# Kernel optimization log

Measured on AMD Instinct MI355X. Metric: run time of the kernel, lower is better.

The kernel has to match this reference:

```python
import jax, jax.numpy as jnp
import numpy as np
from jax import lax

N_GRAPHS = 256
N_NODES = 128      # nodes per graph (fixed-size batching)
N_TPLT = 16
N_TPLT_NODES = 10
N_FEAT = 128
AVG_DEG = 8
EPS = 0.1          # entropic regularization for the GW solver
OUTER_ITERS = 5    # outer mirror-descent (entropic GW) iterations
SINKHORN_ITERS = 20


def setup_inputs() -> dict:
    key = jax.random.key(0)
    k1, k2, k3, k4, k5 = jax.random.split(key, 5)
    x = jax.random.normal(k1, (N_GRAPHS * N_NODES, N_FEAT), jnp.float32)
    # per-graph random edges with global node ids (PyG convention)
    n_e = N_NODES * AVG_DEG
    src = jax.random.randint(k2, (N_GRAPHS, n_e), 0, N_NODES)
    dst = jax.random.randint(k3, (N_GRAPHS, n_e), 0, N_NODES)
    off = (jnp.arange(N_GRAPHS) * N_NODES)[:, None]
    edge_index = jnp.stack([(src + off).reshape(-1), (dst + off).reshape(-1)]).astype(jnp.int32)
    batch = jnp.repeat(jnp.arange(N_GRAPHS, dtype=jnp.int32), N_NODES)
    # template parameters (symmetric uniform adjacencies, normal features, zero q0 -> uniform weights)
    A0 = jax.random.uniform(k4, (N_TPLT, N_TPLT_NODES, N_TPLT_NODES), jnp.float32)
    tplt_adjacencies = 0.5 * (A0 + jnp.swapaxes(A0, 1, 2))
    tplt_features = jax.random.normal(k5, (N_TPLT, N_TPLT_NODES, N_FEAT), jnp.float32)
    q0 = jnp.zeros((N_TPLT, N_TPLT_NODES), jnp.float32)
    return {"x": x, "edge_index": edge_index, "batch": batch,
            "tplt_adjacencies": tplt_adjacencies, "tplt_features": tplt_features, "q0": q0}


def _gw_distances(C1, C2, p, q):
    # C1: [B,N,N] graph adjacencies, C2: [T,M,M] templates, p: [N], q: [T,M]
    # square-loss GW decomposition (Peyre et al.): f1=a^2, f2=b^2, h1=a, h2=2b
    B, N = C1.shape[0], C1.shape[1]
    T, M = C2.shape[0], C2.shape[1]
    f1p = jnp.einsum('bij,j->bi', C1 * C1, p)          # [B,N]
    f2q = jnp.einsum('tij,tj->ti', C2 * C2, q)         # [T,M]
    constC = f1p[:, None, :, None] + f2q[None, :, None, :]  # [B,T,N,M]

    def tens(P):
        # constC - h1(C1) P h2(C2)^T
        cross = jnp.einsum('bik,btkm,tjm->btij', C1, P, 2.0 * C2)
        return constC - cross

    P0 = jnp.broadcast_to(p[None, None, :, None] * q[None, :, None, :], (B, T, N, M))

    def outer(P, _):
        cost = 2.0 * tens(P)                     # GW gradient
        K = jnp.exp(-cost / EPS)                 # [B,T,N,M]
        u0 = jnp.ones((B, T, N), K.dtype)
        v0 = jnp.ones((B, T, M), K.dtype)

        def inner(carry, _):
            u, v = carry
            u = p[None, None, :] / jnp.einsum('btnm,btm->btn', K, v)
            v = q[None, :, :] / jnp.einsum('btnm,btn->btm', K, u)
            return (u, v), None

        (u, v), _ = lax.scan(inner, (u0, v0), None, length=SINKHORN_ITERS)
        P = u[..., :, None] * K * v[..., None, :]
        return P, None

    P, _ = lax.scan(outer, P0, None, length=OUTER_ITERS)
    return jnp.sum(tens(P) * P, axis=(2, 3))     # [B,T]


def reference(x, edge_index, batch, tplt_adjacencies, tplt_features, q0):
    # q = softmax(q0, dim=1): template node weights
    q = jax.nn.softmax(q0, axis=1)
    # dense per-graph adjacency from the sparse edge list
    g = batch[edge_index[0]]
    src = edge_index[0] - g * N_NODES
    dst = edge_index[1] - g * N_NODES
    C1 = jnp.zeros((N_GRAPHS, N_NODES, N_NODES), x.dtype)
    C1 = C1.at[g, src, dst].set(1.0)
    C1 = jnp.maximum(C1, jnp.swapaxes(C1, 1, 2))  # undirected
    p = jnp.full((N_NODES,), 1.0 / N_NODES, x.dtype)  # uniform graph node weights
    # fused=False: pure Gromov-Wasserstein, node features are not used
    return _gw_distances(C1, tplt_adjacencies, p, q)
```

## Files before the change

### kernel.cpp

```cpp
#include <hip/hip_runtime.h>

#define NGRAPH 256
#define NN     128
#define NT     16
#define NM     10
#define OUTER_IT 5
#define SINK_IT  20

#define SC1  28.85390081777927f
#define SC2  57.70780163555854f

typedef unsigned long long u64;
typedef float v2f __attribute__((ext_vector_type(2)));
typedef float v4f __attribute__((ext_vector_type(4)));

static __device__ __forceinline__ v2f pkfma(v2f a, v2f b, v2f c) {
  return __builtin_elementwise_fma(a, b, c);
}
static __device__ __forceinline__ v2f bc2(float s) { return (v2f){s, s}; }

template <int CTRL>
__device__ __forceinline__ float dpp_add(float a) {
  int t = __builtin_amdgcn_update_dpp(0, __float_as_int(a), CTRL, 0xf, 0xf, true);
  return a + __int_as_float(t);
}
__device__ __forceinline__ float allsum32(float x) {
  x = dpp_add<0xB1>(x);
  x = dpp_add<0x4E>(x);
  x = dpp_add<0x141>(x);
  x = dpp_add<0x140>(x);
  int sw = __builtin_amdgcn_ds_swizzle(__float_as_int(x), 0x401F);
  return x + __int_as_float(sw);
}

__global__ __launch_bounds__(64, 2)
void tgw_kernel(const int* __restrict__ ei,
                const float* __restrict__ tadj,
                const float* __restrict__ q0g,
                float* __restrict__ out,
                int E, int ne) {
  const int lane = threadIdx.x;
  const int p    = lane >> 5;
  const int sub  = lane & 31;
  const int b    = blockIdx.x >> 3;
  const int t0   = (blockIdx.x & 7) * 2;

  __shared__ __align__(16) unsigned adj[NN][4];
  __shared__ __align__(16) float Pls[2][NN][12];
  __shared__ __align__(16) v2f C2T[2][NM][6];
  __shared__ float q0s[2][NM];

  for (int i = lane; i < NN * 4; i += 64) (&adj[0][0])[i] = 0u;
  for (int i = lane; i < 2 * NM * 5; i += 64) {
    int tt = i / 50, r = i % 50, m = r / 5, jp = r % 5;
    const float* bp = tadj + (t0 + tt) * NM * NM + m;
    C2T[tt][m][jp] = (v2f){bp[(2 * jp) * NM], bp[(2 * jp + 1) * NM]} * SC2;
  }
  if (lane < 2 * NM) q0s[lane / NM][lane % NM] = q0g[t0 * NM + lane];
  __syncthreads();

  const int* srcp = ei;
  const int* dstp = ei + E;
  const int ebase = b * ne;
  for (int e = lane; e < ne; e += 64) {
    int s = srcp[ebase + e] & (NN - 1);
    int d = dstp[ebase + e] & (NN - 1);
    atomicOr(&adj[s][d >> 5], 1u << (d & 31));
    atomicOr(&adj[d][s >> 5], 1u << (s & 31));
  }
  __syncthreads();

  float qv[NM];
  {
    float mx = q0s[p][0];
    #pragma unroll
    for (int j = 1; j < NM; ++j) mx = fmaxf(mx, q0s[p][j]);
    float s = 0.f;
    #pragma unroll
    for (int j = 0; j < NM; ++j) { qv[j] = __expf(q0s[p][j] - mx); s += qv[j]; }
    float inv = __builtin_amdgcn_rcpf(s);
    #pragma unroll
    for (int j = 0; j < NM; ++j) qv[j] *= inv;
  }
  v2f q2[5];
  #pragma unroll
  for (int jp = 0; jp < 5; ++jp) q2[jp] = (v2f){qv[2 * jp], qv[2 * jp + 1]};

  v2f fq2[5], qC2T[5];
  {
    #pragma unroll
    for (int jp = 0; jp < 5; ++jp) { fq2[jp] = (v2f){0.f, 0.f}; qC2T[jp] = (v2f){0.f, 0.f}; }
    #pragma unroll
    for (int m = 0; m < NM; ++m) {
      v2f qb = bc2(qv[m]);
      #pragma unroll
      for (int jp = 0; jp < 5; ++jp) {
        v2f c = C2T[p][m][jp];
        fq2[jp]  = pkfma(c * c, qb, fq2[jp]);
        qC2T[jp] = pkfma(c, qb, qC2T[jp]);
      }
    }
    const float f = -1.0f / (4.0f * SC1);
    #pragma unroll
    for (int jp = 0; jp < 5; ++jp) fq2[jp] *= f;
  }

  const float pw = 1.0f / 128.0f;
  float f1p[4], m1f1[4];
  #pragma unroll
  for (int c = 0; c < 4; ++c) {
    uint4 mm = *(const uint4*)&adj[sub + 32 * c][0];
    u64 m0 = mm.x | ((u64)mm.y << 32), m1 = mm.z | ((u64)mm.w << 32);
    f1p[c]  = (float)(__popcll(m0) + __popcll(m1)) * pw;
    m1f1[c] = -SC1 * f1p[c];
  }

  const float* Pbase = &Pls[p][0][0];
  auto gatherRow = [&](int r, v2f* S2) {
    uint4 mm = *(const uint4*)&adj[r][0];
    u64 m0 = mm.x | ((u64)mm.y << 32), m1 = mm.z | ((u64)mm.w << 32);
    #pragma unroll
    for (int h = 0; h < 5; ++h) S2[h] = (v2f){0.f, 0.f};
    while (m0) {
      int k = (int)__builtin_ctzll(m0); m0 &= m0 - 1;
      const float* row = Pbase + k * 12;
      v4f A = *(const v4f*)row;
      v4f B = *(const v4f*)(row + 4);
      v2f C = *(const v2f*)(row + 8);
      S2[0] += A.xy; S2[1] += A.zw; S2[2] += B.xy; S2[3] += B.zw; S2[4] += C;
    }
    while (m1) {
      int k = 64 + (int)__builtin_ctzll(m1); m1 &= m1 - 1;
      const float* row = Pbase + k * 12;
      v4f A = *(const v4f*)row;
      v4f B = *(const v4f*)(row + 4);
      v2f C = *(const v2f*)(row + 8);
      S2[0] += A.xy; S2[1] += A.zw; S2[2] += B.xy; S2[3] += B.zw; S2[4] += C;
    }
  };

  auto costFromS = [&](float Sm[4][NM], v2f arg2[4][5]) {
    #pragma unroll
    for (int c = 0; c < 4; ++c) {
      v2f ib = fq2[0] + bc2(m1f1[c]);
      arg2[c][0] = ib;
      #pragma unroll
      for (int jp = 1; jp < 5; ++jp) arg2[c][jp] = fq2[jp] + bc2(m1f1[c]);
    }
    #pragma unroll
    for (int m = 0; m < NM; ++m) {
      v4f X = *(const v4f*)&C2T[p][m][0];
      v4f Y = *(const v4f*)&C2T[p][m][2];
      v2f Z = *(const v2f*)&C2T[p][m][4];
      #pragma unroll
      for (int c = 0; c < 4; ++c) {
        v2f sb = bc2(Sm[c][m]);
        arg2[c][0] = pkfma(sb, X.xy, arg2[c][0]);
        arg2[c][1] = pkfma(sb, X.zw, arg2[c][1]);
        arg2[c][2] = pkfma(sb, Y.xy, arg2[c][2]);
        arg2[c][3] = pkfma(sb, Y.zw, arg2[c][3]);
        arg2[c][4] = pkfma(sb, Z,    arg2[c][4]);
      }
    }
  };

  v2f K2[4][5], v2[5], arg2[4][5];
  float uu[4];

  for (int o = 0; o < OUTER_IT; ++o) {
    if (o == 0) {
      #pragma unroll
      for (int c = 0; c < 4; ++c) {
        v2f fb = bc2(f1p[c]);
        v2f ob = bc2(m1f1[c]);
        #pragma unroll
        for (int jp = 0; jp < 5; ++jp)
          arg2[c][jp] = pkfma(fb, qC2T[jp], fq2[jp] + ob);
      }
    } else {
      float Sm[4][NM];
      #pragma unroll
      for (int c = 0; c < 4; ++c) {
        v2f S2[5];
        gatherRow(sub + 32 * c, S2);
        #pragma unroll
        for (int h = 0; h < 5; ++h) { Sm[c][2 * h] = S2[h].x; Sm[c][2 * h + 1] = S2[h].y; }
      }
      costFromS(Sm, arg2);
    }
    #pragma unroll
    for (int c = 0; c < 4; ++c)
      #pragma unroll
      for (int jp = 0; jp < 5; ++jp)
        K2[c][jp] = (v2f){exp2f(arg2[c][jp].x), exp2f(arg2[c][jp].y)};

    #pragma unroll
    for (int jp = 0; jp < 5; ++jp) v2[jp] = (v2f){1.f, 1.f};
    for (int it = 0; it < SINK_IT; ++it) {
      #pragma unroll
      for (int c = 0; c < 4; ++c) {
        v2f d2 = K2[c][0] * v2[0];
        d2 = pkfma(K2[c][1], v2[1], d2);
        d2 = pkfma(K2[c][2], v2[2], d2);
        d2 = pkfma(K2[c][3], v2[3], d2);
        d2 = pkfma(K2[c][4], v2[4], d2);
        uu[c] = pw * __builtin_amdgcn_rcpf(d2.x + d2.y);
      }
      #pragma unroll
      for (int jp = 0; jp < 5; ++jp) {
        v2f w2 = K2[0][jp] * bc2(uu[0]);
        w2 = pkfma(K2[1][jp], bc2(uu[1]), w2);
        w2 = pkfma(K2[2][jp], bc2(uu[2]), w2);
        w2 = pkfma(K2[3][jp], bc2(uu[3]), w2);
        float cx = allsum32(w2.x);
        float cy = allsum32(w2.y);
        v2[jp] = (v2f){q2[jp].x * __builtin_amdgcn_rcpf(cx),
                       q2[jp].y * __builtin_amdgcn_rcpf(cy)};
      }
    }

    __syncthreads();
    #pragma unroll
    for (int c = 0; c < 4; ++c) {
      v2f ub = bc2(uu[c]);
      v2f x0 = K2[c][0] * ub * v2[0];
      v2f x1 = K2[c][1] * ub * v2[1];
      v2f x2 = K2[c][2] * ub * v2[2];
      v2f x3 = K2[c][3] * ub * v2[3];
      v2f x4 = K2[c][4] * ub * v2[4];
      float* row = &Pls[p][sub + 32 * c][0];
      *(v4f*)row       = (v4f){x0.x, x0.y, x1.x, x1.y};
      *(v4f*)(row + 4) = (v4f){x2.x, x2.y, x3.x, x3.y};
      *(v2f*)(row + 8) = x4;
    }
    __syncthreads();
  }

  float acc = 0.f;
  {
    float Sm[4][NM];
    #pragma unroll
    for (int c = 0; c < 4; ++c) {
      v2f S2[5];
      gatherRow(sub + 32 * c, S2);
      #pragma unroll
      for (int h = 0; h < 5; ++h) { Sm[c][2 * h] = S2[h].x; Sm[c][2 * h + 1] = S2[h].y; }
    }
    costFromS(Sm, arg2);
    const v2f nf = bc2(-1.0f / SC1);
    v2f acc2 = (v2f){0.f, 0.f};
    #pragma unroll
    for (int c = 0; c < 4; ++c) {
      v2f ub = bc2(uu[c]);
      #pragma unroll
      for (int jp = 0; jp < 5; ++jp) {
        v2f Pv = K2[c][jp] * ub * v2[jp];
        acc2 = pkfma(arg2[c][jp] * nf, Pv, acc2);
      }
    }
    acc = acc2.x + acc2.y;
  }
  float total = allsum32(acc);
  if (sub == 0) out[b * NT + t0 + p] = total;
}

extern "C" void kernel_launch(void* const* d_in, const int* in_sizes, int n_in,
                              void* d_out, int out_size, void* d_ws, size_t ws_size,
                              hipStream_t stream) {
  const int* ei   = (const int*)d_in[1];
  const float* c2 = (const float*)d_in[3];
  const float* q0 = (const float*)d_in[5];
  float* out      = (float*)d_out;
  const int E  = in_sizes[1] / 2;
  const int ne = E / NGRAPH;
  tgw_kernel<<<dim3(NGRAPH * 8), dim3(64), 0, stream>>>(ei, c2, q0, out, E, ne);
}
```

Measured before the change: 200.5 us.

## Assign one template per 64-lane block, two rows per lane, wave-wide reduction

Each block previously handled two templates, one per 32-lane half-wave with four rows per lane. Now each block handles one template, each lane owns two rows, and the Sinkhorn column sums use a full 64-lane DPP reduction with readlane. This roughly halves per-lane register state and the serial Sinkhorn work per lane, and launch bounds are raised to allow more waves per SIMD. In exchange it doubles the grid and the per-graph adjacency construction (edge atomics are repeated once per template), and the 64-lane reduction is longer.

```diff
diff --git a/kernel.cpp b/kernel.cpp
--- a/kernel.cpp
+++ b/kernel.cpp
@@ -24,39 +24,42 @@
   int t = __builtin_amdgcn_update_dpp(0, __float_as_int(a), CTRL, 0xf, 0xf, true);
   return a + __int_as_float(t);
 }
-__device__ __forceinline__ float allsum32(float x) {
-  x = dpp_add<0xB1>(x);
-  x = dpp_add<0x4E>(x);
-  x = dpp_add<0x141>(x);
-  x = dpp_add<0x140>(x);
-  int sw = __builtin_amdgcn_ds_swizzle(__float_as_int(x), 0x401F);
-  return x + __int_as_float(sw);
-}
-
-__global__ __launch_bounds__(64, 2)
+__device__ __forceinline__ float allsum64(float x) {
+  x = dpp_add<0x111>(x);
+  x = dpp_add<0x112>(x);
+  x = dpp_add<0x114>(x);
+  x = dpp_add<0x118>(x);
+  x = dpp_add<0x142>(x);
+  x = dpp_add<0x143>(x);
+  return __int_as_float(__builtin_amdgcn_readlane(__float_as_int(x), 63));
+}
+
+__global__ __launch_bounds__(64, 4)
 void tgw_kernel(const int* __restrict__ ei,
                 const float* __restrict__ tadj,
                 const float* __restrict__ q0g,
                 float* __restrict__ out,
                 int E, int ne) {
   const int lane = threadIdx.x;
-  const int p    = lane >> 5;
-  const int sub  = lane & 31;
-  const int b    = blockIdx.x >> 3;
-  const int t0   = (blockIdx.x & 7) * 2;
+  const int b    = blockIdx.x >> 4;
+  const int t    = blockIdx.x & 15;
 
   __shared__ __align__(16) unsigned adj[NN][4];
-  __shared__ __align__(16) float Pls[2][NN][12];
-  __shared__ __align__(16) v2f C2T[2][NM][6];
-  __shared__ float q0s[2][NM];
-
-  for (int i = lane; i < NN * 4; i += 64) (&adj[0][0])[i] = 0u;
-  for (int i = lane; i < 2 * NM * 5; i += 64) {
-    int tt = i / 50, r = i % 50, m = r / 5, jp = r % 5;
-    const float* bp = tadj + (t0 + tt) * NM * NM + m;
-    C2T[tt][m][jp] = (v2f){bp[(2 * jp) * NM], bp[(2 * jp + 1) * NM]} * SC2;
-  }
-  if (lane < 2 * NM) q0s[lane / NM][lane % NM] = q0g[t0 * NM + lane];
+  __shared__ __align__(16) float Pls[NN][12];
+  __shared__ __align__(16) v2f C2T[NM][6];
+  __shared__ float q0s[NM];
+
+  {
+    uint4 z = {0u, 0u, 0u, 0u};
+    ((uint4*)adj)[lane]      = z;
+    ((uint4*)adj)[lane + 64] = z;
+  }
+  if (lane < NM * 5) {
+    int m = lane / 5, jp = lane % 5;
+    const float* bp = tadj + t * NM * NM + m;
+    C2T[m][jp] = (v2f){bp[(2 * jp) * NM], bp[(2 * jp + 1) * NM]} * SC2;
+  }
+  if (lane < NM) q0s[lane] = q0g[t * NM + lane];
   __syncthreads();
 
   const int* srcp = ei;
@@ -70,21 +73,20 @@
   }
   __syncthreads();
 
-  float qv[NM];
-  {
-    float mx = q0s[p][0];
-    #pragma unroll
-    for (int j = 1; j < NM; ++j) mx = fmaxf(mx, q0s[p][j]);
+  v2f q2[5];
+  {
+    float qv[NM];
+    float mx = q0s[0];
+    #pragma unroll
+    for (int j = 1; j < NM; ++j) mx = fmaxf(mx, q0s[j]);
     float s = 0.f;
     #pragma unroll
-    for (int j = 0; j < NM; ++j) { qv[j] = __expf(q0s[p][j] - mx); s += qv[j]; }
+    for (int j = 0; j < NM; ++j) { qv[j] = __expf(q0s[j] - mx); s += qv[j]; }
     float inv = __builtin_amdgcn_rcpf(s);
     #pragma unroll
-    for (int j = 0; j < NM; ++j) qv[j] *= inv;
-  }
-  v2f q2[5];
-  #pragma unroll
-  for (int jp = 0; jp < 5; ++jp) q2[jp] = (v2f){qv[2 * jp], qv[2 * jp + 1]};
+    for (int jp = 0; jp < 5; ++jp)
+      q2[jp] = (v2f){qv[2 * jp] * inv, qv[2 * jp + 1] * inv};
+  }
 
   v2f fq2[5], qC2T[5];
   {
@@ -92,10 +94,11 @@
     for (int jp = 0; jp < 5; ++jp) { fq2[jp] = (v2f){0.f, 0.f}; qC2T[jp] = (v2f){0.f, 0.f}; }
     #pragma unroll
     for (int m = 0; m < NM; ++m) {
-      v2f qb = bc2(qv[m]);
+      float qm = (m & 1) ? q2[m >> 1].y : q2[m >> 1].x;
+      v2f qb = bc2(qm);
       #pragma unroll
       for (int jp = 0; jp < 5; ++jp) {
-        v2f c = C2T[p][m][jp];
+        v2f c = C2T[m][jp];
         fq2[jp]  = pkfma(c * c, qb, fq2[jp]);
         qC2T[jp] = pkfma(c, qb, qC2T[jp]);
       }
@@ -106,16 +109,15 @@
   }
 
   const float pw = 1.0f / 128.0f;
-  float f1p[4], m1f1[4];
+  float f1p[2], m1f1[2];
   #pragma unroll
-  for (int c = 0; c < 4; ++c) {
-    uint4 mm = *(const uint4*)&adj[sub + 32 * c][0];
+  for (int c = 0; c < 2; ++c) {
+    uint4 mm = *(const uint4*)&adj[lane + 64 * c][0];
     u64 m0 = mm.x | ((u64)mm.y << 32), m1 = mm.z | ((u64)mm.w << 32);
     f1p[c]  = (float)(__popcll(m0) + __popcll(m1)) * pw;
     m1f1[c] = -SC1 * f1p[c];
   }
 
-  const float* Pbase = &Pls[p][0][0];
   auto gatherRow = [&](int r, v2f* S2) {
     uint4 mm = *(const uint4*)&adj[r][0];
     u64 m0 = mm.x | ((u64)mm.y << 32), m1 = mm.z | ((u64)mm.w << 32);
@@ -123,7 +125,7 @@
     for (int h = 0; h < 5; ++h) S2[h] = (v2f){0.f, 0.f};
     while (m0) {
       int k = (int)__builtin_ctzll(m0); m0 &= m0 - 1;
-      const float* row = Pbase + k * 12;
+      const float* row = &Pls[k][0];
       v4f A = *(const v4f*)row;
       v4f B = *(const v4f*)(row + 4);
       v2f C = *(const v2f*)(row + 8);
@@ -131,7 +133,7 @@
     }
     while (m1) {
       int k = 64 + (int)__builtin_ctzll(m1); m1 &= m1 - 1;
-      const float* row = Pbase + k * 12;
+      const float* row = &Pls[k][0];
       v4f A = *(const v4f*)row;
       v4f B = *(const v4f*)(row + 4);
       v2f C = *(const v2f*)(row + 8);
@@ -139,22 +141,20 @@
     }
   };
 
-  auto costFromS = [&](float Sm[4][NM], v2f arg2[4][5]) {
-    #pragma unroll
-    for (int c = 0; c < 4; ++c) {
-      v2f ib = fq2[0] + bc2(m1f1[c]);
-      arg2[c][0] = ib;
-      #pragma unroll
-      for (int jp = 1; jp < 5; ++jp) arg2[c][jp] = fq2[jp] + bc2(m1f1[c]);
-    }
+  auto costFromS = [&](v2f Sm[2][5], v2f arg2[2][5]) {
+    #pragma unroll
+    for (int c = 0; c < 2; ++c)
+      #pragma unroll
+      for (int jp = 0; jp < 5; ++jp) arg2[c][jp] = fq2[jp] + bc2(m1f1[c]);
     #pragma unroll
     for (int m = 0; m < NM; ++m) {
-      v4f X = *(const v4f*)&C2T[p][m][0];
-      v4f Y = *(const v4f*)&C2T[p][m][2];
-      v2f Z = *(const v2f*)&C2T[p][m][4];
-      #pragma unroll
-      for (int c = 0; c < 4; ++c) {
-        v2f sb = bc2(Sm[c][m]);
+      v4f X = *(const v4f*)&C2T[m][0];
+      v4f Y = *(const v4f*)&C2T[m][2];
+      v2f Z = *(const v2f*)&C2T[m][4];
+      #pragma unroll
+      for (int c = 0; c < 2; ++c) {
+        float sv = (m & 1) ? Sm[c][m >> 1].y : Sm[c][m >> 1].x;
+        v2f sb = bc2(sv);
         arg2[c][0] = pkfma(sb, X.xy, arg2[c][0]);
         arg2[c][1] = pkfma(sb, X.zw, arg2[c][1]);
         arg2[c][2] = pkfma(sb, Y.xy, arg2[c][2]);
@@ -164,13 +164,13 @@
     }
   };
 
-  v2f K2[4][5], v2[5], arg2[4][5];
-  float uu[4];
+  v2f K2[2][5], v2[5], arg2[2][5];
+  float uu[2];
 
   for (int o = 0; o < OUTER_IT; ++o) {
     if (o == 0) {
       #pragma unroll
-      for (int c = 0; c < 4; ++c) {
+      for (int c = 0; c < 2; ++c) {
         v2f fb = bc2(f1p[c]);
         v2f ob = bc2(m1f1[c]);
         #pragma unroll
@@ -178,18 +178,13 @@
           arg2[c][jp] = pkfma(fb, qC2T[jp], fq2[jp] + ob);
       }
     } else {
-      float Sm[4][NM];
-      #pragma unroll
-      for (int c = 0; c < 4; ++c) {
-        v2f S2[5];
-        gatherRow(sub + 32 * c, S2);
-        #pragma unroll
-        for (int h = 0; h < 5; ++h) { Sm[c][2 * h] = S2[h].x; Sm[c][2 * h + 1] = S2[h].y; }
-      }
+      v2f Sm[2][5];
+      gatherRow(lane,      Sm[0]);
+      gatherRow(lane + 64, Sm[1]);
       costFromS(Sm, arg2);
     }
     #pragma unroll
-    for (int c = 0; c < 4; ++c)
+    for (int c = 0; c < 2; ++c)
       #pragma unroll
       for (int jp = 0; jp < 5; ++jp)
         K2[c][jp] = (v2f){exp2f(arg2[c][jp].x), exp2f(arg2[c][jp].y)};
@@ -198,7 +193,7 @@
     for (int jp = 0; jp < 5; ++jp) v2[jp] = (v2f){1.f, 1.f};
     for (int it = 0; it < SINK_IT; ++it) {
       #pragma unroll
-      for (int c = 0; c < 4; ++c) {
+      for (int c = 0; c < 2; ++c) {
         v2f d2 = K2[c][0] * v2[0];
         d2 = pkfma(K2[c][1], v2[1], d2);
         d2 = pkfma(K2[c][2], v2[2], d2);
@@ -210,10 +205,8 @@
       for (int jp = 0; jp < 5; ++jp) {
         v2f w2 = K2[0][jp] * bc2(uu[0]);
         w2 = pkfma(K2[1][jp], bc2(uu[1]), w2);
-        w2 = pkfma(K2[2][jp], bc2(uu[2]), w2);
-        w2 = pkfma(K2[3][jp], bc2(uu[3]), w2);
-        float cx = allsum32(w2.x);
-        float cy = allsum32(w2.y);
+        float cx = allsum64(w2.x);
+        float cy = allsum64(w2.y);
         v2[jp] = (v2f){q2[jp].x * __builtin_amdgcn_rcpf(cx),
                        q2[jp].y * __builtin_amdgcn_rcpf(cy)};
       }
@@ -221,14 +214,14 @@
 
     __syncthreads();
     #pragma unroll
-    for (int c = 0; c < 4; ++c) {
+    for (int c = 0; c < 2; ++c) {
       v2f ub = bc2(uu[c]);
       v2f x0 = K2[c][0] * ub * v2[0];
       v2f x1 = K2[c][1] * ub * v2[1];
       v2f x2 = K2[c][2] * ub * v2[2];
       v2f x3 = K2[c][3] * ub * v2[3];
       v2f x4 = K2[c][4] * ub * v2[4];
-      float* row = &Pls[p][sub + 32 * c][0];
+      float* row = &Pls[lane + 64 * c][0];
       *(v4f*)row       = (v4f){x0.x, x0.y, x1.x, x1.y};
       *(v4f*)(row + 4) = (v4f){x2.x, x2.y, x3.x, x3.y};
       *(v2f*)(row + 8) = x4;
@@ -236,21 +229,16 @@
     __syncthreads();
   }
 
-  float acc = 0.f;
-  {
-    float Sm[4][NM];
-    #pragma unroll
-    for (int c = 0; c < 4; ++c) {
-      v2f S2[5];
-      gatherRow(sub + 32 * c, S2);
-      #pragma unroll
-      for (int h = 0; h < 5; ++h) { Sm[c][2 * h] = S2[h].x; Sm[c][2 * h + 1] = S2[h].y; }
-    }
+  float acc;
+  {
+    v2f Sm[2][5];
+    gatherRow(lane,      Sm[0]);
+    gatherRow(lane + 64, Sm[1]);
     costFromS(Sm, arg2);
     const v2f nf = bc2(-1.0f / SC1);
     v2f acc2 = (v2f){0.f, 0.f};
     #pragma unroll
-    for (int c = 0; c < 4; ++c) {
+    for (int c = 0; c < 2; ++c) {
       v2f ub = bc2(uu[c]);
       #pragma unroll
       for (int jp = 0; jp < 5; ++jp) {
@@ -260,8 +248,8 @@
     }
     acc = acc2.x + acc2.y;
   }
-  float total = allsum32(acc);
-  if (sub == 0) out[b * NT + t0 + p] = total;
+  float total = allsum64(acc);
+  if (lane == 0) out[b * NT + t] = total;
 }
 
 extern "C" void kernel_launch(void* const* d_in, const int* in_sizes, int n_in,
@@ -273,5 +261,5 @@
   float* out      = (float*)d_out;
   const int E  = in_sizes[1] / 2;
   const int ne = E / NGRAPH;
-  tgw_kernel<<<dim3(NGRAPH * 8), dim3(64), 0, stream>>>(ei, c2, q0, out, E, ne);
-}
+  tgw_kernel<<<dim3(NGRAPH * NT), dim3(64), 0, stream>>>(ei, c2, q0, out, E, ne);
+}
```

After: 222.2 us. +10.8%, slower.

## Fold q into Sinkhorn kernel copy, pair bitmask gathers, use raw exp2

Applied to the files above, without the earlier changes.

Rescales the Sinkhorn variables by keeping a second kernel matrix Kh2 = K*q*128, so each iteration's v update is a bare reciprocal and the u update drops the pw multiply. It also interleaves the two 64-bit adjacency halves in the sparse row gather to expose more independent LDS loads, and switches exp2f to the hardware exp2 builtin. The cost is doubled register use for the K matrices, which could lower occupancy or cause spills, and small numerical differences.

```diff
diff --git a/kernel.cpp b/kernel.cpp
--- a/kernel.cpp
+++ b/kernel.cpp
@@ -82,9 +82,15 @@
     #pragma unroll
     for (int j = 0; j < NM; ++j) qv[j] *= inv;
   }
-  v2f q2[5];
+  v2f q2[5], qt2[5], vh0[5];
+  const float pw = 1.0f / 128.0f;
   #pragma unroll
-  for (int jp = 0; jp < 5; ++jp) q2[jp] = (v2f){qv[2 * jp], qv[2 * jp + 1]};
+  for (int jp = 0; jp < 5; ++jp) {
+    q2[jp]  = (v2f){qv[2 * jp], qv[2 * jp + 1]};
+    qt2[jp] = q2[jp] * 128.0f;
+    vh0[jp] = (v2f){pw * __builtin_amdgcn_rcpf(q2[jp].x),
+                    pw * __builtin_amdgcn_rcpf(q2[jp].y)};
+  }
 
   v2f fq2[5], qC2T[5];
   {
@@ -92,7 +98,8 @@
     for (int jp = 0; jp < 5; ++jp) { fq2[jp] = (v2f){0.f, 0.f}; qC2T[jp] = (v2f){0.f, 0.f}; }
     #pragma unroll
     for (int m = 0; m < NM; ++m) {
-      v2f qb = bc2(qv[m]);
+      float qm = (m & 1) ? q2[m >> 1].y : q2[m >> 1].x;
+      v2f qb = bc2(qm);
       #pragma unroll
       for (int jp = 0; jp < 5; ++jp) {
         v2f c = C2T[p][m][jp];
@@ -105,7 +112,6 @@
     for (int jp = 0; jp < 5; ++jp) fq2[jp] *= f;
   }
 
-  const float pw = 1.0f / 128.0f;
   float f1p[4], m1f1[4];
   #pragma unroll
   for (int c = 0; c < 4; ++c) {
@@ -121,32 +127,35 @@
     u64 m0 = mm.x | ((u64)mm.y << 32), m1 = mm.z | ((u64)mm.w << 32);
     #pragma unroll
     for (int h = 0; h < 5; ++h) S2[h] = (v2f){0.f, 0.f};
+    while (m0 && m1) {
+      int k0 = (int)__builtin_ctzll(m0); m0 &= m0 - 1;
+      int k1 = 64 + (int)__builtin_ctzll(m1); m1 &= m1 - 1;
+      const float* r0 = Pbase + k0 * 12;
+      const float* r1 = Pbase + k1 * 12;
+      v4f A0 = *(const v4f*)r0; v4f B0 = *(const v4f*)(r0 + 4); v2f C0 = *(const v2f*)(r0 + 8);
+      v4f A1 = *(const v4f*)r1; v4f B1 = *(const v4f*)(r1 + 4); v2f C1 = *(const v2f*)(r1 + 8);
+      S2[0] += A0.xy; S2[1] += A0.zw; S2[2] += B0.xy; S2[3] += B0.zw; S2[4] += C0;
+      S2[0] += A1.xy; S2[1] += A1.zw; S2[2] += B1.xy; S2[3] += B1.zw; S2[4] += C1;
+    }
     while (m0) {
       int k = (int)__builtin_ctzll(m0); m0 &= m0 - 1;
       const float* row = Pbase + k * 12;
-      v4f A = *(const v4f*)row;
-      v4f B = *(const v4f*)(row + 4);
-      v2f C = *(const v2f*)(row + 8);
+      v4f A = *(const v4f*)row; v4f B = *(const v4f*)(row + 4); v2f C = *(const v2f*)(row + 8);
       S2[0] += A.xy; S2[1] += A.zw; S2[2] += B.xy; S2[3] += B.zw; S2[4] += C;
     }
     while (m1) {
       int k = 64 + (int)__builtin_ctzll(m1); m1 &= m1 - 1;
       const float* row = Pbase + k * 12;
-      v4f A = *(const v4f*)row;
-      v4f B = *(const v4f*)(row + 4);
-      v2f C = *(const v2f*)(row + 8);
+      v4f A = *(const v4f*)row; v4f B = *(const v4f*)(row + 4); v2f C = *(const v2f*)(row + 8);
       S2[0] += A.xy; S2[1] += A.zw; S2[2] += B.xy; S2[3] += B.zw; S2[4] += C;
     }
   };
 
-  auto costFromS = [&](float Sm[4][NM], v2f arg2[4][5]) {
-    #pragma unroll
-    for (int c = 0; c < 4; ++c) {
-      v2f ib = fq2[0] + bc2(m1f1[c]);
-      arg2[c][0] = ib;
-      #pragma unroll
-      for (int jp = 1; jp < 5; ++jp) arg2[c][jp] = fq2[jp] + bc2(m1f1[c]);
-    }
+  auto costFromS = [&](v2f Sm[4][5], v2f arg2[4][5]) {
+    #pragma unroll
+    for (int c = 0; c < 4; ++c)
+      #pragma unroll
+      for (int jp = 0; jp < 5; ++jp) arg2[c][jp] = fq2[jp] + bc2(m1f1[c]);
     #pragma unroll
     for (int m = 0; m < NM; ++m) {
       v4f X = *(const v4f*)&C2T[p][m][0];
@@ -154,7 +163,8 @@
       v2f Z = *(const v2f*)&C2T[p][m][4];
       #pragma unroll
       for (int c = 0; c < 4; ++c) {
-        v2f sb = bc2(Sm[c][m]);
+        float sv = (m & 1) ? Sm[c][m >> 1].y : Sm[c][m >> 1].x;
+        v2f sb = bc2(sv);
         arg2[c][0] = pkfma(sb, X.xy, arg2[c][0]);
         arg2[c][1] = pkfma(sb, X.zw, arg2[c][1]);
         arg2[c][2] = pkfma(sb, Y.xy, arg2[c][2]);
@@ -164,7 +174,7 @@
     }
   };
 
-  v2f K2[4][5], v2[5], arg2[4][5];
+  v2f K2[4][5], Kh2[4][5], vh[5], arg2[4][5];
   float uu[4];
 
   for (int o = 0; o < OUTER_IT; ++o) {
@@ -178,33 +188,31 @@
           arg2[c][jp] = pkfma(fb, qC2T[jp], fq2[jp] + ob);
       }
     } else {
-      float Sm[4][NM];
+      v2f Sm[4][5];
+      #pragma unroll
+      for (int c = 0; c < 4; ++c) gatherRow(sub + 32 * c, Sm[c]);
+      costFromS(Sm, arg2);
+    }
+    #pragma unroll
+    for (int c = 0; c < 4; ++c)
+      #pragma unroll
+      for (int jp = 0; jp < 5; ++jp) {
+        K2[c][jp] = (v2f){__builtin_amdgcn_exp2f(arg2[c][jp].x),
+                          __builtin_amdgcn_exp2f(arg2[c][jp].y)};
+        Kh2[c][jp] = K2[c][jp] * qt2[jp];
+      }
+
+    #pragma unroll
+    for (int jp = 0; jp < 5; ++jp) vh[jp] = vh0[jp];
+    for (int it = 0; it < SINK_IT; ++it) {
       #pragma unroll
       for (int c = 0; c < 4; ++c) {
-        v2f S2[5];
-        gatherRow(sub + 32 * c, S2);
-        #pragma unroll
-        for (int h = 0; h < 5; ++h) { Sm[c][2 * h] = S2[h].x; Sm[c][2 * h + 1] = S2[h].y; }
-      }
-      costFromS(Sm, arg2);
-    }
-    #pragma unroll
-    for (int c = 0; c < 4; ++c)
-      #pragma unroll
-      for (int jp = 0; jp < 5; ++jp)
-        K2[c][jp] = (v2f){exp2f(arg2[c][jp].x), exp2f(arg2[c][jp].y)};
-
-    #pragma unroll
-    for (int jp = 0; jp < 5; ++jp) v2[jp] = (v2f){1.f, 1.f};
-    for (int it = 0; it < SINK_IT; ++it) {
-      #pragma unroll
-      for (int c = 0; c < 4; ++c) {
-        v2f d2 = K2[c][0] * v2[0];
-        d2 = pkfma(K2[c][1], v2[1], d2);
-        d2 = pkfma(K2[c][2], v2[2], d2);
-        d2 = pkfma(K2[c][3], v2[3], d2);
-        d2 = pkfma(K2[c][4], v2[4], d2);
-        uu[c] = pw * __builtin_amdgcn_rcpf(d2.x + d2.y);
+        v2f d2 = Kh2[c][0] * vh[0];
+        d2 = pkfma(Kh2[c][1], vh[1], d2);
+        d2 = pkfma(Kh2[c][2], vh[2], d2);
+        d2 = pkfma(Kh2[c][3], vh[3], d2);
+        d2 = pkfma(Kh2[c][4], vh[4], d2);
+        uu[c] = __builtin_amdgcn_rcpf(d2.x + d2.y);
       }
       #pragma unroll
       for (int jp = 0; jp < 5; ++jp) {
@@ -214,20 +222,19 @@
         w2 = pkfma(K2[3][jp], bc2(uu[3]), w2);
         float cx = allsum32(w2.x);
         float cy = allsum32(w2.y);
-        v2[jp] = (v2f){q2[jp].x * __builtin_amdgcn_rcpf(cx),
-                       q2[jp].y * __builtin_amdgcn_rcpf(cy)};
+        vh[jp] = (v2f){__builtin_amdgcn_rcpf(cx), __builtin_amdgcn_rcpf(cy)};
       }
     }
 
     __syncthreads();
     #pragma unroll
     for (int c = 0; c < 4; ++c) {
-      v2f ub = bc2(uu[c]);
-      v2f x0 = K2[c][0] * ub * v2[0];
-      v2f x1 = K2[c][1] * ub * v2[1];
-      v2f x2 = K2[c][2] * ub * v2[2];
-      v2f x3 = K2[c][3] * ub * v2[3];
-      v2f x4 = K2[c][4] * ub * v2[4];
+      v2f ub = bc2(pw * uu[c]);
+      v2f x0 = Kh2[c][0] * ub * vh[0];
+      v2f x1 = Kh2[c][1] * ub * vh[1];
+      v2f x2 = Kh2[c][2] * ub * vh[2];
+      v2f x3 = Kh2[c][3] * ub * vh[3];
+      v2f x4 = Kh2[c][4] * ub * vh[4];
       float* row = &Pls[p][sub + 32 * c][0];
       *(v4f*)row       = (v4f){x0.x, x0.y, x1.x, x1.y};
       *(v4f*)(row + 4) = (v4f){x2.x, x2.y, x3.x, x3.y};
@@ -236,25 +243,20 @@
     __syncthreads();
   }
 
-  float acc = 0.f;
+  float acc;
   {
-    float Sm[4][NM];
-    #pragma unroll
-    for (int c = 0; c < 4; ++c) {
-      v2f S2[5];
-      gatherRow(sub + 32 * c, S2);
-      #pragma unroll
-      for (int h = 0; h < 5; ++h) { Sm[c][2 * h] = S2[h].x; Sm[c][2 * h + 1] = S2[h].y; }
-    }
+    v2f Sm[4][5];
+    #pragma unroll
+    for (int c = 0; c < 4; ++c) gatherRow(sub + 32 * c, Sm[c]);
     costFromS(Sm, arg2);
     const v2f nf = bc2(-1.0f / SC1);
     v2f acc2 = (v2f){0.f, 0.f};
     #pragma unroll
     for (int c = 0; c < 4; ++c) {
-      v2f ub = bc2(uu[c]);
-      #pragma unroll
-      for (int jp = 0; jp < 5; ++jp) {
-        v2f Pv = K2[c][jp] * ub * v2[jp];
+      v2f ub = bc2(pw * uu[c]);
+      #pragma unroll
+      for (int jp = 0; jp < 5; ++jp) {
+        v2f Pv = Kh2[c][jp] * ub * vh[jp];
         acc2 = pkfma(arg2[c][jp] * nf, Pv, acc2);
       }
     }
```

After: 206.0 us. 2.8% more time.
